# Performance work log

Hardware: AMD Instinct MI355X
Metric: run time of the kernel (lower is better)

## Reference

```python
import jax, jax.numpy as jnp
import numpy as np

N, E, IN_CH, HID, EDGE_DIM, L, G = 50000, 800000, 64, 128, 16, 3, 256

def _bn(h, g, b):
    # BatchNorm1d in training mode (biased batch variance), eps=1e-5
    m = h.mean(0)
    v = ((h - m) ** 2).mean(0)
    return (h - m) * jax.lax.rsqrt(v + 1e-5) * g + b

def setup_inputs() -> dict:
    key = jax.random.key(0)
    ks = jax.random.split(key, 24)
    s = 0.05
    inp = {
        'x': jax.random.normal(ks[0], (N, IN_CH), jnp.float32),
        'edge_attr': jax.random.uniform(ks[1], (E, EDGE_DIM), jnp.float32),
        'src': jax.random.randint(ks[2], (E,), 0, N, jnp.int32),
        'dst': jax.random.randint(ks[3], (E,), 0, N, jnp.int32),
        'batch': jnp.sort(jax.random.randint(ks[4], (N,), 0, G, jnp.int32)),
        'Wp': jax.random.normal(ks[5], (IN_CH, HID), jnp.float32) * s,
        'bp': jnp.zeros((HID,), jnp.float32),
        'conv_We': jax.random.normal(ks[6], (L, EDGE_DIM, HID), jnp.float32) * s,
        'conv_be': jnp.zeros((L, HID), jnp.float32),
        'conv_W1': jax.random.normal(ks[7], (L, HID, HID), jnp.float32) * s,
        'conv_b1': jnp.zeros((L, HID), jnp.float32),
        'conv_g1': jnp.ones((L, HID), jnp.float32),
        'conv_bt1': jnp.zeros((L, HID), jnp.float32),
        'conv_W2': jax.random.normal(ks[8], (L, HID, HID), jnp.float32) * s,
        'conv_b2': jnp.zeros((L, HID), jnp.float32),
        'bn_g': jnp.ones((L, HID), jnp.float32),
        'bn_b': jnp.zeros((L, HID), jnp.float32),
        'head_W1': jax.random.normal(ks[9], (HID * L * 2, HID), jnp.float32) * s,
        'head_b1': jnp.zeros((HID,), jnp.float32),
        'head_g': jnp.ones((HID,), jnp.float32),
        'head_bt': jnp.zeros((HID,), jnp.float32),
        'head_W2': jax.random.normal(ks[10], (HID, 1), jnp.float32) * s,
        'head_b2': jnp.zeros((1,), jnp.float32),
    }
    return inp

def reference(x, edge_attr, src, dst, batch, Wp, bp, conv_We, conv_be, conv_W1, conv_b1,
              conv_g1, conv_bt1, conv_W2, conv_b2, bn_g, bn_b, head_W1, head_b1,
              head_g, head_bt, head_W2, head_b2):
    n = x.shape[0]
    h = x @ Wp + bp  # [N, HID]
    outs = []
    for l in range(L):
        # GINEConv: msg = ReLU(x_src + lin(edge_attr)); sum-aggregate to dst; (1+eps)*x + agg, eps=0
        ee = edge_attr @ conv_We[l] + conv_be[l]          # [E, HID]
        msg = jax.nn.relu(h[src] + ee)                     # [E, HID]
        agg = jax.ops.segment_sum(msg, dst, num_segments=n)
        t = h + agg
        t = t @ conv_W1[l] + conv_b1[l]
        t = jax.nn.relu(_bn(t, conv_g1[l], conv_bt1[l]))
        t = t @ conv_W2[l] + conv_b2[l]
        h = jax.nn.relu(_bn(t, bn_g[l], bn_b[l]))          # outer BN + ReLU (dropout = identity, eval)
        outs.append(h)
    xj = jnp.concatenate(outs, axis=-1)                    # JK 'cat' -> [N, 3*HID]
    cnt = jax.ops.segment_sum(jnp.ones((n,), xj.dtype), batch, num_segments=G)
    z_mean = jax.ops.segment_sum(xj, batch, num_segments=G) / jnp.clip(cnt, 1.0)[:, None]
    z_max = jax.ops.segment_max(xj, batch, num_segments=G)
    z = jnp.concatenate([z_mean, z_max], axis=-1)          # [G, 6*HID]
    z = z @ head_W1 + head_b1
    z = jax.nn.relu(_bn(z, head_g, head_bt))
    return (z @ head_W2 + head_b2).squeeze(-1)             # [G]
```

## Files before the change

### kernel.cpp

```cpp
#include <hip/hip_runtime.h>
#include <hip/hip_bf16.h>

#define HID 128
#define EDIM 16

typedef float v4f __attribute__((ext_vector_type(4)));
typedef float v2f __attribute__((ext_vector_type(2)));
typedef short s8v __attribute__((ext_vector_type(8)));
typedef float f4v __attribute__((ext_vector_type(4)));

#define MFMA_BF16(a, b, c) __builtin_amdgcn_mfma_f32_16x16x32_bf16((a), (b), (c), 0, 0, 0)

__device__ __forceinline__ unsigned short bf16_rne(float v)
{
    unsigned u = __builtin_bit_cast(unsigned, v);
    return (unsigned short)((u + 0x7fffu + ((u >> 16) & 1u)) >> 16);
}

__device__ __forceinline__ unsigned pack2(float lo, float hi)
{
    return (unsigned)bf16_rne(lo) | ((unsigned)bf16_rne(hi) << 16);
}

__device__ __forceinline__ float bflo(unsigned u) { return __builtin_bit_cast(float, u << 16); }
__device__ __forceinline__ float bfhi(unsigned u) { return __builtin_bit_cast(float, u & 0xffff0000u); }

__device__ __forceinline__ v2f unpack2(unsigned u)
{
    v2f r; r.x = bflo(u); r.y = bfhi(u); return r;
}

__device__ __forceinline__ void split_bf16(float v, unsigned short& h, unsigned short& l)
{
    unsigned u = __builtin_bit_cast(unsigned, v);
    unsigned hu = (u + 0x7fffu + ((u >> 16) & 1u)) >> 16;
    h = (unsigned short)hu;
    float hf = __builtin_bit_cast(float, hu << 16);
    l = bf16_rne(v - hf);
}

__device__ __forceinline__ v2f vmax0(v2f a)
{
    v2f r; r.x = fmaxf(a.x, 0.f); r.y = fmaxf(a.y, 0.f); return r;
}

__global__ void hist_kernel(const int* __restrict__ dst, int* __restrict__ deg, int E)
{
    int e = blockIdx.x * 256 + threadIdx.x;
    if (e < E) atomicAdd(&deg[dst[e]], 1);
}

__global__ void block_sum_kernel(const int* __restrict__ deg, int* __restrict__ bsum, int Nn)
{
    int i = blockIdx.x * 256 + threadIdx.x;
    int v = (i < Nn) ? deg[i] : 0;
#pragma unroll
    for (int off = 32; off > 0; off >>= 1) v += __shfl_down(v, off, 64);
    __shared__ int ws[4];
    if ((threadIdx.x & 63) == 0) ws[threadIdx.x >> 6] = v;
    __syncthreads();
    if (threadIdx.x == 0) bsum[blockIdx.x] = ws[0] + ws[1] + ws[2] + ws[3];
}

__global__ void bsum_scan_kernel(int* bsum, int nb, int* total_out)
{
    __shared__ int sh[256];
    int tid = threadIdx.x;
    int v = (tid < nb) ? bsum[tid] : 0;
    sh[tid] = v;
    __syncthreads();
    for (int off = 1; off < 256; off <<= 1) {
        int tv = (tid >= off) ? sh[tid - off] : 0;
        __syncthreads();
        sh[tid] += tv;
        __syncthreads();
    }
    if (tid < nb) bsum[tid] = sh[tid] - v;
    if (tid == 255) *total_out = sh[255];
}

__global__ void block_scan_kernel(const int* __restrict__ deg, const int* __restrict__ bsum,
                                  int* __restrict__ row_start, int* __restrict__ cursor, int Nn)
{
    __shared__ int sh[256];
    int tid = threadIdx.x;
    int i = blockIdx.x * 256 + tid;
    int v = (i < Nn) ? deg[i] : 0;
    sh[tid] = v;
    __syncthreads();
    for (int off = 1; off < 256; off <<= 1) {
        int tv = (tid >= off) ? sh[tid - off] : 0;
        __syncthreads();
        sh[tid] += tv;
        __syncthreads();
    }
    if (i < Nn) {
        int excl = sh[tid] - v + bsum[blockIdx.x];
        row_start[i] = excl;
        cursor[i] = excl;
    }
}

__global__ void scatter_kernel(const int* __restrict__ src, const int* __restrict__ dst,
                               int* cursor, int* __restrict__ perm,
                               int* __restrict__ src_perm, int E)
{
    int e = blockIdx.x * 256 + threadIdx.x;
    if (e >= E) return;
    int pos = atomicAdd(&cursor[dst[e]], 1);
    perm[pos] = e;
    src_perm[pos] = src[e];
}

__global__ void gather_ea_kernel(const float* __restrict__ ea, const int* __restrict__ perm,
                                 float* __restrict__ ea_perm, int E)
{
    int idx = blockIdx.x * 256 + threadIdx.x;
    int p = idx >> 2, c = (idx & 3) * 4;
    if (p >= E) return;
    int e = perm[p];
    *(float4*)&ea_perm[(size_t)p * EDIM + c] = *(const float4*)&ea[(size_t)e * EDIM + c];
}

__global__ void prep_weights(const float* __restrict__ Wp, const float* __restrict__ W1,
                             const float* __restrict__ W2, unsigned short* __restrict__ out)
{
    int idx = blockIdx.x * 256 + threadIdx.x;
    if (idx < 8192) {
        int n = idx >> 6, k = idx & 63;
        unsigned short h, l;
        split_bf16(Wp[k * 128 + n], h, l);
        out[idx] = h;
        out[8192 + idx] = l;
    } else {
        int j = idx - 8192;
        if (j >= 6 * 16384) return;
        int m2 = j >> 14;
        int r = j & 16383;
        int n = r >> 7, k = r & 127;
        int l = m2 >> 1;
        const float* Wsrc = (m2 & 1) ? (W2 + l * 16384) : (W1 + l * 16384);
        unsigned short h, lo;
        split_bf16(Wsrc[k * 128 + n], h, lo);
        int base = 16384 + m2 * 32768;
        out[base + r] = h;
        out[base + 16384 + r] = lo;
    }
}

__device__ __forceinline__ void matvp(const v4f& a0, const v4f& a1,
                                      const v4f& a2, const v4f& a3,
                                      const v2f* __restrict__ w, v2f& m)
{
    m += w[0] * a0.x;  m += w[1] * a0.y;  m += w[2] * a0.z;  m += w[3] * a0.w;
    m += w[4] * a1.x;  m += w[5] * a1.y;  m += w[6] * a1.z;  m += w[7] * a1.w;
    m += w[8] * a2.x;  m += w[9] * a2.y;  m += w[10] * a2.z; m += w[11] * a2.w;
    m += w[12] * a3.x; m += w[13] * a3.y; m += w[14] * a3.z; m += w[15] * a3.w;
}

template<bool GATH>
__global__ __launch_bounds__(256, 8) void aggregate_kernel(
    const unsigned short* __restrict__ h16, const float* __restrict__ eaG,
    const int* __restrict__ perm, const int* __restrict__ src_perm,
    const int* __restrict__ row_start,
    const float* __restrict__ We, const float* __restrict__ be,
    float* __restrict__ t, int Nn)
{
    int tid = threadIdx.x;
    int lane = tid & 63;
    int c = lane * 2;
    v2f w[16];
#pragma unroll
    for (int k = 0; k < 16; ++k) w[k] = *(const v2f*)&We[k * HID + c];
    v2f bj = *(const v2f*)&be[c];
    int node = blockIdx.x * 4 + (tid >> 6);
    if (node >= Nn) return;
    const unsigned* __restrict__ hw = (const unsigned*)h16 + lane;
    v2f acc = unpack2(hw[(unsigned)node << 6]);
    int p0 = __builtin_amdgcn_readfirstlane(row_start[node]);
    int p1 = __builtin_amdgcn_readfirstlane(row_start[node + 1]);
    int p = p0;
    int s0 = 0, s1 = 0, s2 = 0, s3 = 0;
    if (p + 4 <= p1) { s0 = src_perm[p]; s1 = src_perm[p + 1]; s2 = src_perm[p + 2]; s3 = src_perm[p + 3]; }
    while (p + 4 <= p1) {
        int np = p + 4;
        int t0 = 0, t1 = 0, t2 = 0, t3 = 0;
        if (np + 4 <= p1) { t0 = src_perm[np]; t1 = src_perm[np + 1]; t2 = src_perm[np + 2]; t3 = src_perm[np + 3]; }
        unsigned hu0 = hw[(unsigned)s0 << 6];
        unsigned hu1 = hw[(unsigned)s1 << 6];
        unsigned hu2 = hw[(unsigned)s2 << 6];
        unsigned hu3 = hw[(unsigned)s3 << 6];
        int q0, q1, q2, q3;
        if (GATH) { q0 = p; q1 = p + 1; q2 = p + 2; q3 = p + 3; }
        else      { q0 = perm[p]; q1 = perm[p + 1]; q2 = perm[p + 2]; q3 = perm[p + 3]; }
        const v4f* e0 = (const v4f*)(eaG + (size_t)(unsigned)q0 * EDIM);
        const v4f* e1 = (const v4f*)(eaG + (size_t)(unsigned)q1 * EDIM);
        const v4f* e2 = (const v4f*)(eaG + (size_t)(unsigned)q2 * EDIM);
        const v4f* e3 = (const v4f*)(eaG + (size_t)(unsigned)q3 * EDIM);
        v4f a00 = e0[0], a01 = e0[1], a02 = e0[2], a03 = e0[3];
        v4f a10 = e1[0], a11 = e1[1], a12 = e1[2], a13 = e1[3];
        v4f a20 = e2[0], a21 = e2[1], a22 = e2[2], a23 = e2[3];
        v4f a30 = e3[0], a31 = e3[1], a32 = e3[2], a33 = e3[3];
        v2f m0 = bj + unpack2(hu0), m1 = bj + unpack2(hu1);
        v2f m2 = bj + unpack2(hu2), m3 = bj + unpack2(hu3);
        matvp(a00, a01, a02, a03, w, m0);
        matvp(a10, a11, a12, a13, w, m1);
        matvp(a20, a21, a22, a23, w, m2);
        matvp(a30, a31, a32, a33, w, m3);
        acc += vmax0(m0) + vmax0(m1) + vmax0(m2) + vmax0(m3);
        p = np;
        s0 = t0; s1 = t1; s2 = t2; s3 = t3;
    }
    for (; p < p1; ++p) {
        int s = src_perm[p];
        int q = GATH ? p : perm[p];
        const v4f* e0 = (const v4f*)(eaG + (size_t)(unsigned)q * EDIM);
        v4f a0 = e0[0], a1 = e0[1], a2 = e0[2], a3 = e0[3];
        v2f m0 = bj + unpack2(hw[(unsigned)s << 6]);
        matvp(a0, a1, a2, a3, w, m0);
        acc += vmax0(m0);
    }
    *(v2f*)(t + ((unsigned)node << 7) + c) = acc;
}

#define LPAD 40

template<int K, bool PRE_BN, bool POST_STATS, bool OUT_BF16>
__global__ __launch_bounds__(256) void gemm_mfma(
    const float* __restrict__ A, const unsigned short* __restrict__ Wh,
    const unsigned short* __restrict__ Wl, const float* __restrict__ bias,
    const float* __restrict__ preStats, const float* __restrict__ preG, const float* __restrict__ preB,
    void* __restrict__ Cout, float* __restrict__ postStats, int Nrows, float invN)
{
    __shared__ __align__(16) unsigned short Ah[128 * LPAD], Al[128 * LPAD];
    __shared__ __align__(16) unsigned short Bh[128 * LPAD], Bl[128 * LPAD];
    __shared__ float sc[PRE_BN ? K : 1], sb[PRE_BN ? K : 1];
    int tid = threadIdx.x;
    int rbase = blockIdx.x * 128;
    if (PRE_BN) {
        if (tid < K) {
            float mean = preStats[tid] * invN;
            float var = preStats[K + tid] * invN - mean * mean;
            float rstd = rsqrtf(var + 1e-5f);
            float g = preG[tid];
            sc[tid] = rstd * g;
            sb[tid] = preB[tid] - mean * rstd * g;
        }
        __syncthreads();
    }
    int w = tid >> 6, nl = tid & 15, q = (tid >> 4) & 3;
    f4v acc[2][8];
#pragma unroll
    for (int mt = 0; mt < 2; ++mt)
#pragma unroll
        for (int nt = 0; nt < 8; ++nt)
#pragma unroll
            for (int r = 0; r < 4; ++r) acc[mt][nt][r] = 0.f;

    for (int ks = 0; ks < K / 32; ++ks) {
        int k0 = ks * 32;
        if (ks) __syncthreads();
#pragma unroll
        for (int i = 0; i < 4; ++i) {
            int cidx = tid + i * 256;
            int m = cidx >> 3, k4 = (cidx & 7) * 4;
            int gr = rbase + m;
            float4 v = make_float4(0.f, 0.f, 0.f, 0.f);
            if (gr < Nrows) v = *(const float4*)&A[(size_t)gr * K + k0 + k4];
            if (PRE_BN) {
                v.x = fmaxf(v.x * sc[k0 + k4]     + sb[k0 + k4],     0.f);
                v.y = fmaxf(v.y * sc[k0 + k4 + 1] + sb[k0 + k4 + 1], 0.f);
                v.z = fmaxf(v.z * sc[k0 + k4 + 2] + sb[k0 + k4 + 2], 0.f);
                v.w = fmaxf(v.w * sc[k0 + k4 + 3] + sb[k0 + k4 + 3], 0.f);
            }
            unsigned short h0, l0, h1, l1, h2, l2, h3, l3;
            split_bf16(v.x, h0, l0); split_bf16(v.y, h1, l1);
            split_bf16(v.z, h2, l2); split_bf16(v.w, h3, l3);
            uint2 hp, lp;
            hp.x = (unsigned)h0 | ((unsigned)h1 << 16); hp.y = (unsigned)h2 | ((unsigned)h3 << 16);
            lp.x = (unsigned)l0 | ((unsigned)l1 << 16); lp.y = (unsigned)l2 | ((unsigned)l3 << 16);
            *(uint2*)&Ah[m * LPAD + k4] = hp;
            *(uint2*)&Al[m * LPAD + k4] = lp;
        }
#pragma unroll
        for (int i = 0; i < 2; ++i) {
            int g = tid + i * 256;
            int n = g >> 2, kq = (g & 3) * 8;
            uint4 hv = *(const uint4*)&Wh[(size_t)n * K + k0 + kq];
            uint4 lv = *(const uint4*)&Wl[(size_t)n * K + k0 + kq];
            *(uint4*)&Bh[n * LPAD + kq] = hv;
            *(uint4*)&Bl[n * LPAD + kq] = lv;
        }
        __syncthreads();
        s8v ah0 = *(const s8v*)&Ah[(w * 32 + nl) * LPAD + q * 8];
        s8v ah1 = *(const s8v*)&Ah[(w * 32 + 16 + nl) * LPAD + q * 8];
        s8v al0 = *(const s8v*)&Al[(w * 32 + nl) * LPAD + q * 8];
        s8v al1 = *(const s8v*)&Al[(w * 32 + 16 + nl) * LPAD + q * 8];
#pragma unroll
        for (int nt = 0; nt < 8; ++nt) {
            s8v bh = *(const s8v*)&Bh[(nt * 16 + nl) * LPAD + q * 8];
            s8v bl = *(const s8v*)&Bl[(nt * 16 + nl) * LPAD + q * 8];
            acc[0][nt] = MFMA_BF16(ah0, bh, acc[0][nt]);
            acc[0][nt] = MFMA_BF16(ah0, bl, acc[0][nt]);
            acc[0][nt] = MFMA_BF16(al0, bh, acc[0][nt]);
            acc[1][nt] = MFMA_BF16(ah1, bh, acc[1][nt]);
            acc[1][nt] = MFMA_BF16(ah1, bl, acc[1][nt]);
            acc[1][nt] = MFMA_BF16(al1, bh, acc[1][nt]);
        }
    }
    __syncthreads();

    float* Cf = (float*)Cout;
    unsigned short* Ch = (unsigned short*)Cout;
    float* redS = (float*)Ah;
    float* redQ = (float*)Al;
#pragma unroll
    for (int nt = 0; nt < 8; ++nt) {
        int col = nt * 16 + nl;
        float bcol = bias[col];
        float sv = 0.f, qv = 0.f;
#pragma unroll
        for (int mt = 0; mt < 2; ++mt) {
#pragma unroll
            for (int r = 0; r < 4; ++r) {
                int grow = rbase + w * 32 + mt * 16 + q * 4 + r;
                if (grow < Nrows) {
                    float o = acc[mt][nt][r] + bcol;
                    if (OUT_BF16) Ch[(size_t)grow * HID + col] = bf16_rne(o);
                    else          Cf[(size_t)grow * HID + col] = o;
                    if (POST_STATS) { sv += o; qv += o * o; }
                }
            }
        }
        if (POST_STATS) {
            sv += __shfl_down(sv, 32, 64); sv += __shfl_down(sv, 16, 64);
            qv += __shfl_down(qv, 32, 64); qv += __shfl_down(qv, 16, 64);
            if ((tid & 63) < 16) { redS[w * 128 + col] = sv; redQ[w * 128 + col] = qv; }
        }
    }
    if (POST_STATS) {
        __syncthreads();
        if (tid < 128) {
            float S = redS[tid] + redS[128 + tid] + redS[256 + tid] + redS[384 + tid];
            float Q = redQ[tid] + redQ[128 + tid] + redQ[256 + tid] + redQ[384 + tid];
            atomicAdd(&postStats[tid], S);
            atomicAdd(&postStats[128 + tid], Q);
        }
    }
}

__global__ void bn_apply_pool(const float* __restrict__ X, unsigned short* __restrict__ h16,
                              const float* __restrict__ stats, const float* __restrict__ g,
                              const float* __restrict__ b, const int* __restrict__ starts,
                              float* __restrict__ z, int l, float invN)
{
    int gph = blockIdx.x;
    int tid = threadIdx.x;
    int ch4 = (tid & 31) * 4, wk = tid >> 5;
    float sc[4], sh[4];
#pragma unroll
    for (int u = 0; u < 4; ++u) {
        int j = ch4 + u;
        float mean = stats[j] * invN;
        float var = stats[128 + j] * invN - mean * mean;
        float rstd = rsqrtf(var + 1e-5f);
        float gg = g[j];
        sc[u] = rstd * gg;
        sh[u] = b[j] - mean * rstd * gg;
    }
    int s = starts[gph], e = starts[gph + 1];
    float4 sum = make_float4(0.f, 0.f, 0.f, 0.f);
    float4 mx = make_float4(0.f, 0.f, 0.f, 0.f);
    unsigned* hv32 = (unsigned*)h16;
    for (int n = s + wk; n < e; n += 16) {
        float4 v = *(const float4*)&X[(size_t)n * HID + ch4];
        v.x = fmaxf(v.x * sc[0] + sh[0], 0.f);
        v.y = fmaxf(v.y * sc[1] + sh[1], 0.f);
        v.z = fmaxf(v.z * sc[2] + sh[2], 0.f);
        v.w = fmaxf(v.w * sc[3] + sh[3], 0.f);
        uint2 pk;
        pk.x = pack2(v.x, v.y);
        pk.y = pack2(v.z, v.w);
        *(uint2*)&hv32[(size_t)n * 64 + (ch4 >> 1)] = pk;
        sum.x += v.x; sum.y += v.y; sum.z += v.z; sum.w += v.w;
        mx.x = fmaxf(mx.x, v.x); mx.y = fmaxf(mx.y, v.y);
        mx.z = fmaxf(mx.z, v.z); mx.w = fmaxf(mx.w, v.w);
    }
    __shared__ float ls[16 * 128], lm[16 * 128];
    *(float4*)&ls[wk * 128 + ch4] = sum;
    *(float4*)&lm[wk * 128 + ch4] = mx;
    __syncthreads();
    if (tid < 128) {
        float S = 0.f, M = 0.f;
#pragma unroll
        for (int k = 0; k < 16; ++k) {
            S += ls[k * 128 + tid];
            M = fmaxf(M, lm[k * 128 + tid]);
        }
        float cnt = (float)(e - s);
        z[(size_t)gph * 768 + l * 128 + tid] = S / fmaxf(cnt, 1.f);
        z[(size_t)gph * 768 + 384 + l * 128 + tid] = M;
    }
}

__global__ void starts_kernel(const int* __restrict__ batch, int* __restrict__ starts,
                              int Nn, int Gn)
{
    int g = blockIdx.x * blockDim.x + threadIdx.x;
    if (g > Gn) return;
    int lo = 0, hi = Nn;
    while (lo < hi) { int mid = (lo + hi) >> 1; if (batch[mid] < g) lo = mid + 1; else hi = mid; }
    starts[g] = lo;
}

__global__ void head_gemm1(const float* __restrict__ z, const float* __restrict__ W,
                           const float* __restrict__ bias, float* __restrict__ zr,
                           float* __restrict__ msums)
{
    __shared__ __align__(16) float zl[768];
    int g = blockIdx.x, j = threadIdx.x;
    for (int i = j; i < 768; i += 128) zl[i] = z[(size_t)g * 768 + i];
    __syncthreads();
    float acc = bias[j];
    for (int k = 0; k < 768; k += 4) {
        float4 a4 = *(const float4*)&zl[k];
        acc += a4.x * W[k * 128 + j] + a4.y * W[(k + 1) * 128 + j]
             + a4.z * W[(k + 2) * 128 + j] + a4.w * W[(k + 3) * 128 + j];
    }
    zr[(size_t)g * 128 + j] = acc;
    atomicAdd(&msums[j], acc);
    atomicAdd(&msums[128 + j], acc * acc);
}

__global__ void head_final(const float* __restrict__ zr, const float* __restrict__ msums,
                           const float* __restrict__ hg, const float* __restrict__ hb,
                           const float* __restrict__ W2, const float* __restrict__ b2,
                           float* __restrict__ out, float invG)
{
    int g = blockIdx.x, j = threadIdx.x;
    float mean = msums[j] * invG;
    float var = msums[128 + j] * invG - mean * mean;
    float rstd = rsqrtf(var + 1e-5f);
    float v = zr[(size_t)g * 128 + j];
    v = (v - mean) * rstd * hg[j] + hb[j];
    v = fmaxf(v, 0.f);
    float p = v * W2[j];
#pragma unroll
    for (int off = 32; off > 0; off >>= 1) p += __shfl_down(p, off, 64);
    __shared__ float partial[2];
    if ((j & 63) == 0) partial[j >> 6] = p;
    __syncthreads();
    if (j == 0) out[g] = partial[0] + partial[1] + b2[0];
}

extern "C" void kernel_launch(void* const* d_in, const int* in_sizes, int n_in,
                              void* d_out, int out_size, void* d_ws, size_t ws_size,
                              hipStream_t stream)
{
    const float* x         = (const float*)d_in[0];
    const float* edge_attr = (const float*)d_in[1];
    const int*   src       = (const int*)d_in[2];
    const int*   dst       = (const int*)d_in[3];
    const int*   batch     = (const int*)d_in[4];
    const float* Wp        = (const float*)d_in[5];
    const float* bp        = (const float*)d_in[6];
    const float* conv_We   = (const float*)d_in[7];
    const float* conv_be   = (const float*)d_in[8];
    const float* conv_W1   = (const float*)d_in[9];
    const float* conv_b1   = (const float*)d_in[10];
    const float* conv_g1   = (const float*)d_in[11];
    const float* conv_bt1  = (const float*)d_in[12];
    const float* conv_W2   = (const float*)d_in[13];
    const float* conv_b2   = (const float*)d_in[14];
    const float* bn_g      = (const float*)d_in[15];
    const float* bn_b      = (const float*)d_in[16];
    const float* head_W1   = (const float*)d_in[17];
    const float* head_b1   = (const float*)d_in[18];
    const float* head_g    = (const float*)d_in[19];
    const float* head_bt   = (const float*)d_in[20];
    const float* head_W2   = (const float*)d_in[21];
    const float* head_b2   = (const float*)d_in[22];

    const int N = in_sizes[4];
    const int E = in_sizes[2];
    const int G = out_size;
    const int L = 3;

    float* t        = (float*)d_ws;
    unsigned short* h16 = (unsigned short*)(t + (size_t)N * HID);
    float* z        = (float*)(h16 + (size_t)N * HID);
    float* zr       = z + (size_t)G * 768;
    float* statsAll = zr + (size_t)G * HID;
    int*   deg      = (int*)(statsAll + 7 * 256);
    int*   starts   = deg + N;
    int*   row_start= starts + (G + 1);
    int*   cursor   = row_start + (N + 1);
    int*   bsum     = cursor + N;
    int*   src_perm = bsum + 256;
    int*   perm     = src_perm + E;
    unsigned short* wt = (unsigned short*)(perm + E);
    size_t base_end = (size_t)((char*)(wt + 212992) - (char*)d_ws);
    size_t ea_off = (base_end + 63) & ~(size_t)63;
    bool gath = (ea_off + (size_t)E * EDIM * sizeof(float)) <= ws_size;
    float* ea_perm = (float*)((char*)d_ws + ea_off);
    float* msums = statsAll + 6 * 256;

    (void)n_in;

    const float invN = 1.0f / (float)N;
    const float invG = 1.0f / (float)G;
    const int nb = (N + 255) / 256;
    const int gemmBlocks = (N + 127) / 128;

    (void)hipMemsetAsync(statsAll, 0, 7 * 256 * sizeof(float) + (size_t)N * sizeof(int), stream);
    hist_kernel<<<(E + 255) / 256, 256, 0, stream>>>(dst, deg, E);
    block_sum_kernel<<<nb, 256, 0, stream>>>(deg, bsum, N);
    bsum_scan_kernel<<<1, 256, 0, stream>>>(bsum, nb, &row_start[N]);
    block_scan_kernel<<<nb, 256, 0, stream>>>(deg, bsum, row_start, cursor, N);
    scatter_kernel<<<(E + 255) / 256, 256, 0, stream>>>(src, dst, cursor, perm, src_perm, E);
    if (gath)
        gather_ea_kernel<<<(E * 4 + 255) / 256, 256, 0, stream>>>(edge_attr, perm, ea_perm, E);
    starts_kernel<<<1, 512, 0, stream>>>(batch, starts, N, G);
    prep_weights<<<(8192 + 6 * 16384 + 255) / 256, 256, 0, stream>>>(Wp, conv_W1, conv_W2, wt);

    const unsigned short* Wp_hi = wt;
    const unsigned short* Wp_lo = wt + 8192;

    gemm_mfma<64, false, false, true><<<gemmBlocks, 256, 0, stream>>>(
        x, Wp_hi, Wp_lo, bp, nullptr, nullptr, nullptr, h16, nullptr, N, invN);

    for (int l = 0; l < L; ++l) {
        float* sI = statsAll + l * 512;
        float* sO = sI + 256;
        const unsigned short* W1hi = wt + 16384 + (size_t)(2 * l) * 32768;
        const unsigned short* W1lo = W1hi + 16384;
        const unsigned short* W2hi = wt + 16384 + (size_t)(2 * l + 1) * 32768;
        const unsigned short* W2lo = W2hi + 16384;
        if (gath)
            aggregate_kernel<true><<<(N + 3) / 4, 256, 0, stream>>>(
                h16, ea_perm, perm, src_perm, row_start,
                conv_We + (size_t)l * EDIM * HID, conv_be + l * HID, t, N);
        else
            aggregate_kernel<false><<<(N + 3) / 4, 256, 0, stream>>>(
                h16, edge_attr, perm, src_perm, row_start,
                conv_We + (size_t)l * EDIM * HID, conv_be + l * HID, t, N);
        gemm_mfma<128, false, true, false><<<gemmBlocks, 256, 0, stream>>>(
            t, W1hi, W1lo, conv_b1 + l * HID,
            nullptr, nullptr, nullptr, t, sI, N, invN);
        gemm_mfma<128, true, true, false><<<gemmBlocks, 256, 0, stream>>>(
            t, W2hi, W2lo, conv_b2 + l * HID,
            sI, conv_g1 + l * HID, conv_bt1 + l * HID, t, sO, N, invN);
        bn_apply_pool<<<G, 512, 0, stream>>>(
            t, h16, sO, bn_g + l * HID, bn_b + l * HID, starts, z, l, invN);
    }

    head_gemm1<<<G, 128, 0, stream>>>(z, head_W1, head_b1, zr, msums);
    head_final<<<G, 128, 0, stream>>>(zr, msums, head_g, head_bt, head_W2, head_b2,
                                      (float*)d_out, invG);
}
```

Measured before the change: 675.1 us.

## Stage per-wave edge attributes and source indices in LDS for aggregation

The aggregation kernel now loads each node's edge_attr rows and source indices in chunks of 64 into per-wave shared memory with coalesced float4 loads. Previously every lane re-read the same edge_attr rows as broadcast global loads. The inner loop reads edge features from LDS and prefetches neighbour h values two groups ahead through the staged index buffer. It adds about 20KB of LDS per block and lowers the occupancy hint from 8 to 4. No barriers are used, so correctness relies on implicit wave-level ordering of the LDS writes and reads.

```diff
diff --git a/kernel.cpp b/kernel.cpp
--- a/kernel.cpp
+++ b/kernel.cpp
@@ -159,66 +159,114 @@
 }
 
 template<bool GATH>
-__global__ __launch_bounds__(256, 8) void aggregate_kernel(
+__global__ __launch_bounds__(256, 4) void aggregate_kernel(
     const unsigned short* __restrict__ h16, const float* __restrict__ eaG,
     const int* __restrict__ perm, const int* __restrict__ src_perm,
     const int* __restrict__ row_start,
     const float* __restrict__ We, const float* __restrict__ be,
-    float* __restrict__ t, int Nn)
-{
+    float* __restrict__ t, int Nn, int Etot)
+{
+    __shared__ __align__(16) float ea_s[4][64 * EDIM];
+    __shared__ __align__(16) int   src_s[4][72];
+    __shared__ __align__(16) int   perm_s[4][64];
+
     int tid = threadIdx.x;
-    int lane = tid & 63;
+    int w = tid >> 6, lane = tid & 63;
     int c = lane * 2;
-    v2f w[16];
-#pragma unroll
-    for (int k = 0; k < 16; ++k) w[k] = *(const v2f*)&We[k * HID + c];
+    v2f wv[16];
+#pragma unroll
+    for (int k = 0; k < 16; ++k) wv[k] = *(const v2f*)&We[k * HID + c];
     v2f bj = *(const v2f*)&be[c];
-    int node = blockIdx.x * 4 + (tid >> 6);
+    int node = blockIdx.x * 4 + w;
     if (node >= Nn) return;
     const unsigned* __restrict__ hw = (const unsigned*)h16 + lane;
     v2f acc = unpack2(hw[(unsigned)node << 6]);
     int p0 = __builtin_amdgcn_readfirstlane(row_start[node]);
     int p1 = __builtin_amdgcn_readfirstlane(row_start[node + 1]);
-    int p = p0;
-    int s0 = 0, s1 = 0, s2 = 0, s3 = 0;
-    if (p + 4 <= p1) { s0 = src_perm[p]; s1 = src_perm[p + 1]; s2 = src_perm[p + 2]; s3 = src_perm[p + 3]; }
-    while (p + 4 <= p1) {
-        int np = p + 4;
-        int t0 = 0, t1 = 0, t2 = 0, t3 = 0;
-        if (np + 4 <= p1) { t0 = src_perm[np]; t1 = src_perm[np + 1]; t2 = src_perm[np + 2]; t3 = src_perm[np + 3]; }
-        unsigned hu0 = hw[(unsigned)s0 << 6];
-        unsigned hu1 = hw[(unsigned)s1 << 6];
-        unsigned hu2 = hw[(unsigned)s2 << 6];
-        unsigned hu3 = hw[(unsigned)s3 << 6];
-        int q0, q1, q2, q3;
-        if (GATH) { q0 = p; q1 = p + 1; q2 = p + 2; q3 = p + 3; }
-        else      { q0 = perm[p]; q1 = perm[p + 1]; q2 = perm[p + 2]; q3 = perm[p + 3]; }
-        const v4f* e0 = (const v4f*)(eaG + (size_t)(unsigned)q0 * EDIM);
-        const v4f* e1 = (const v4f*)(eaG + (size_t)(unsigned)q1 * EDIM);
-        const v4f* e2 = (const v4f*)(eaG + (size_t)(unsigned)q2 * EDIM);
-        const v4f* e3 = (const v4f*)(eaG + (size_t)(unsigned)q3 * EDIM);
-        v4f a00 = e0[0], a01 = e0[1], a02 = e0[2], a03 = e0[3];
-        v4f a10 = e1[0], a11 = e1[1], a12 = e1[2], a13 = e1[3];
-        v4f a20 = e2[0], a21 = e2[1], a22 = e2[2], a23 = e2[3];
-        v4f a30 = e3[0], a31 = e3[1], a32 = e3[2], a33 = e3[3];
-        v2f m0 = bj + unpack2(hu0), m1 = bj + unpack2(hu1);
-        v2f m2 = bj + unpack2(hu2), m3 = bj + unpack2(hu3);
-        matvp(a00, a01, a02, a03, w, m0);
-        matvp(a10, a11, a12, a13, w, m1);
-        matvp(a20, a21, a22, a23, w, m2);
-        matvp(a30, a31, a32, a33, w, m3);
-        acc += vmax0(m0) + vmax0(m1) + vmax0(m2) + vmax0(m3);
-        p = np;
-        s0 = t0; s1 = t1; s2 = t2; s3 = t3;
-    }
-    for (; p < p1; ++p) {
-        int s = src_perm[p];
-        int q = GATH ? p : perm[p];
-        const v4f* e0 = (const v4f*)(eaG + (size_t)(unsigned)q * EDIM);
-        v4f a0 = e0[0], a1 = e0[1], a2 = e0[2], a3 = e0[3];
-        v2f m0 = bj + unpack2(hw[(unsigned)s << 6]);
-        matvp(a0, a1, a2, a3, w, m0);
-        acc += vmax0(m0);
+    float* eas = ea_s[w];
+    int*   srcs = src_s[w];
+    int*   prms = perm_s[w];
+
+    for (int cs = p0; cs < p1; cs += 64) {
+        int cn = p1 - cs; if (cn > 64) cn = 64;
+
+        srcs[lane] = (cs + lane < p1) ? src_perm[cs + lane] : 0;
+        if (lane < 8) srcs[64 + lane] = 0;
+
+        if (GATH) {
+#pragma unroll
+            for (int tp = 0; tp < 4; ++tp) {
+                if (tp * 16 < cn) {
+                    int e = cs + tp * 16 + (lane >> 2);
+                    float4 v = make_float4(0.f, 0.f, 0.f, 0.f);
+                    if (e < Etot) v = *(const float4*)&eaG[(size_t)e * EDIM + (lane & 3) * 4];
+                    *(float4*)&eas[tp * 256 + lane * 4] = v;
+                }
+            }
+        } else {
+            prms[lane] = (cs + lane < p1) ? perm[cs + lane] : 0;
+#pragma unroll
+            for (int tp = 0; tp < 4; ++tp) {
+                if (tp * 16 < cn) {
+                    int el = tp * 16 + (lane >> 2);
+                    int pv = prms[el];
+                    float4 v = *(const float4*)&eaG[(size_t)(unsigned)pv * EDIM + (lane & 3) * 4];
+                    *(float4*)&eas[tp * 256 + lane * 4] = v;
+                }
+            }
+        }
+
+        int ngroups = (cn + 3) >> 2;
+        int4 scur = *(const int4*)&srcs[0];
+        int4 snxt = *(const int4*)&srcs[4];
+        unsigned hu0 = hw[(unsigned)scur.x << 6];
+        unsigned hu1 = hw[(unsigned)scur.y << 6];
+        unsigned hu2 = hw[(unsigned)scur.z << 6];
+        unsigned hu3 = hw[(unsigned)scur.w << 6];
+        for (int g = 0; g < ngroups; ++g) {
+            int4 s2 = *(const int4*)&srcs[(g + 2) * 4];
+            unsigned hn0 = hw[(unsigned)snxt.x << 6];
+            unsigned hn1 = hw[(unsigned)snxt.y << 6];
+            unsigned hn2 = hw[(unsigned)snxt.z << 6];
+            unsigned hn3 = hw[(unsigned)snxt.w << 6];
+            int eb = g * 4;
+            v4f a0 = *(const v4f*)&eas[(eb + 0) * EDIM + 0];
+            v4f a1 = *(const v4f*)&eas[(eb + 0) * EDIM + 4];
+            v4f a2 = *(const v4f*)&eas[(eb + 0) * EDIM + 8];
+            v4f a3 = *(const v4f*)&eas[(eb + 0) * EDIM + 12];
+            v2f m0 = bj + unpack2(hu0);
+            matvp(a0, a1, a2, a3, wv, m0);
+            a0 = *(const v4f*)&eas[(eb + 1) * EDIM + 0];
+            a1 = *(const v4f*)&eas[(eb + 1) * EDIM + 4];
+            a2 = *(const v4f*)&eas[(eb + 1) * EDIM + 8];
+            a3 = *(const v4f*)&eas[(eb + 1) * EDIM + 12];
+            v2f m1 = bj + unpack2(hu1);
+            matvp(a0, a1, a2, a3, wv, m1);
+            a0 = *(const v4f*)&eas[(eb + 2) * EDIM + 0];
+            a1 = *(const v4f*)&eas[(eb + 2) * EDIM + 4];
+            a2 = *(const v4f*)&eas[(eb + 2) * EDIM + 8];
+            a3 = *(const v4f*)&eas[(eb + 2) * EDIM + 12];
+            v2f m2 = bj + unpack2(hu2);
+            matvp(a0, a1, a2, a3, wv, m2);
+            a0 = *(const v4f*)&eas[(eb + 3) * EDIM + 0];
+            a1 = *(const v4f*)&eas[(eb + 3) * EDIM + 4];
+            a2 = *(const v4f*)&eas[(eb + 3) * EDIM + 8];
+            a3 = *(const v4f*)&eas[(eb + 3) * EDIM + 12];
+            v2f m3 = bj + unpack2(hu3);
+            matvp(a0, a1, a2, a3, wv, m3);
+
+            v2f r0 = vmax0(m0), r1 = vmax0(m1), r2 = vmax0(m2), r3 = vmax0(m3);
+            if (eb + 4 <= cn) {
+                acc += (r0 + r1) + (r2 + r3);
+            } else {
+                if (eb + 0 < cn) acc += r0;
+                if (eb + 1 < cn) acc += r1;
+                if (eb + 2 < cn) acc += r2;
+                if (eb + 3 < cn) acc += r3;
+            }
+            hu0 = hn0; hu1 = hn1; hu2 = hn2; hu3 = hn3;
+            scur = snxt; snxt = s2;
+        }
     }
     *(v2f*)(t + ((unsigned)node << 7) + c) = acc;
 }
@@ -539,11 +587,11 @@
         if (gath)
             aggregate_kernel<true><<<(N + 3) / 4, 256, 0, stream>>>(
                 h16, ea_perm, perm, src_perm, row_start,
-                conv_We + (size_t)l * EDIM * HID, conv_be + l * HID, t, N);
+                conv_We + (size_t)l * EDIM * HID, conv_be + l * HID, t, N, E);
         else
             aggregate_kernel<false><<<(N + 3) / 4, 256, 0, stream>>>(
                 h16, edge_attr, perm, src_perm, row_start,
-                conv_We + (size_t)l * EDIM * HID, conv_be + l * HID, t, N);
+                conv_We + (size_t)l * EDIM * HID, conv_be + l * HID, t, N, E);
         gemm_mfma<128, false, true, false><<<gemmBlocks, 256, 0, stream>>>(
             t, W1hi, W1lo, conv_b1 + l * HID,
             nullptr, nullptr, nullptr, t, sI, N, invN);
```

New measurement: 716.8 us. +6.2%, slower.

## Compute edge linear in aggregation with bf16 MFMA instead of scalar FMAs

Applied to the files above, without the earlier changes.

Replaces the per-lane scalar 16x128 edge-attribute projection in the GINE aggregation with MFMA 16x16x32 bf16 ops over 16-edge chunks. Edge attributes are split into hi/lo bf16 pairs, the bias is folded in as an extra K column, and the weights are pre-transposed to bf16 by a new prep kernel. It then gathers source features as scalar bf16 loads, masks padded rows, and reduces partial sums across lanes through shared memory. The aim is to cut VALU work per edge. In exchange it adds narrower gathers, wasted MFMA work on low-degree nodes, a lower occupancy hint, and bf16 rounding of the weights.

```diff
diff --git a/kernel.cpp b/kernel.cpp
--- a/kernel.cpp
+++ b/kernel.cpp
@@ -37,11 +37,6 @@
     h = (unsigned short)hu;
     float hf = __builtin_bit_cast(float, hu << 16);
     l = bf16_rne(v - hf);
-}
-
-__device__ __forceinline__ v2f vmax0(v2f a)
-{
-    v2f r; r.x = fmaxf(a.x, 0.f); r.y = fmaxf(a.y, 0.f); return r;
 }
 
 __global__ void hist_kernel(const int* __restrict__ dst, int* __restrict__ deg, int E)
@@ -148,79 +143,119 @@
     }
 }
 
-__device__ __forceinline__ void matvp(const v4f& a0, const v4f& a1,
-                                      const v4f& a2, const v4f& a3,
-                                      const v2f* __restrict__ w, v2f& m)
-{
-    m += w[0] * a0.x;  m += w[1] * a0.y;  m += w[2] * a0.z;  m += w[3] * a0.w;
-    m += w[4] * a1.x;  m += w[5] * a1.y;  m += w[6] * a1.z;  m += w[7] * a1.w;
-    m += w[8] * a2.x;  m += w[9] * a2.y;  m += w[10] * a2.z; m += w[11] * a2.w;
-    m += w[12] * a3.x; m += w[13] * a3.y; m += w[14] * a3.z; m += w[15] * a3.w;
+__global__ void prep_wet(const float* __restrict__ We, const float* __restrict__ be,
+                         unsigned short* __restrict__ out)
+{
+    int idx = blockIdx.x * 256 + threadIdx.x;
+    if (idx >= 3 * 4096) return;
+    int l = idx >> 12, r = idx & 4095, ch = r >> 5, k = r & 31;
+    float v = 0.f;
+    if (k < 16)       v = We[l * EDIM * HID + k * HID + ch];
+    else if (k == 16) v = be[l * HID + ch];
+    out[idx] = bf16_rne(v);
 }
 
 template<bool GATH>
-__global__ __launch_bounds__(256, 8) void aggregate_kernel(
+__global__ __launch_bounds__(256, 4) void aggregate_kernel(
     const unsigned short* __restrict__ h16, const float* __restrict__ eaG,
     const int* __restrict__ perm, const int* __restrict__ src_perm,
-    const int* __restrict__ row_start,
-    const float* __restrict__ We, const float* __restrict__ be,
+    const int* __restrict__ row_start, const unsigned short* __restrict__ WeT,
     float* __restrict__ t, int Nn)
 {
+    __shared__ float fin_s[4][132];
     int tid = threadIdx.x;
-    int lane = tid & 63;
-    int c = lane * 2;
-    v2f w[16];
-#pragma unroll
-    for (int k = 0; k < 16; ++k) w[k] = *(const v2f*)&We[k * HID + c];
-    v2f bj = *(const v2f*)&be[c];
-    int node = blockIdx.x * 4 + (tid >> 6);
+    int w = tid >> 6, lane = tid & 63;
+    int qq = lane >> 4, m16 = lane & 15;
+
+    int node = blockIdx.x * 4 + w;
     if (node >= Nn) return;
-    const unsigned* __restrict__ hw = (const unsigned*)h16 + lane;
-    v2f acc = unpack2(hw[(unsigned)node << 6]);
+
+    s8v bf[8];
+#pragma unroll
+    for (int nt = 0; nt < 8; ++nt)
+        bf[nt] = *(const s8v*)&WeT[(size_t)((nt * 16 + m16) * 32 + qq * 8)];
+
+    v2f selfpair = unpack2(((const unsigned*)h16)[((unsigned)node << 6) + lane]);
+
     int p0 = __builtin_amdgcn_readfirstlane(row_start[node]);
     int p1 = __builtin_amdgcn_readfirstlane(row_start[node + 1]);
-    int p = p0;
-    int s0 = 0, s1 = 0, s2 = 0, s3 = 0;
-    if (p + 4 <= p1) { s0 = src_perm[p]; s1 = src_perm[p + 1]; s2 = src_perm[p + 2]; s3 = src_perm[p + 3]; }
-    while (p + 4 <= p1) {
-        int np = p + 4;
-        int t0 = 0, t1 = 0, t2 = 0, t3 = 0;
-        if (np + 4 <= p1) { t0 = src_perm[np]; t1 = src_perm[np + 1]; t2 = src_perm[np + 2]; t3 = src_perm[np + 3]; }
-        unsigned hu0 = hw[(unsigned)s0 << 6];
-        unsigned hu1 = hw[(unsigned)s1 << 6];
-        unsigned hu2 = hw[(unsigned)s2 << 6];
-        unsigned hu3 = hw[(unsigned)s3 << 6];
-        int q0, q1, q2, q3;
-        if (GATH) { q0 = p; q1 = p + 1; q2 = p + 2; q3 = p + 3; }
-        else      { q0 = perm[p]; q1 = perm[p + 1]; q2 = perm[p + 2]; q3 = perm[p + 3]; }
-        const v4f* e0 = (const v4f*)(eaG + (size_t)(unsigned)q0 * EDIM);
-        const v4f* e1 = (const v4f*)(eaG + (size_t)(unsigned)q1 * EDIM);
-        const v4f* e2 = (const v4f*)(eaG + (size_t)(unsigned)q2 * EDIM);
-        const v4f* e3 = (const v4f*)(eaG + (size_t)(unsigned)q3 * EDIM);
-        v4f a00 = e0[0], a01 = e0[1], a02 = e0[2], a03 = e0[3];
-        v4f a10 = e1[0], a11 = e1[1], a12 = e1[2], a13 = e1[3];
-        v4f a20 = e2[0], a21 = e2[1], a22 = e2[2], a23 = e2[3];
-        v4f a30 = e3[0], a31 = e3[1], a32 = e3[2], a33 = e3[3];
-        v2f m0 = bj + unpack2(hu0), m1 = bj + unpack2(hu1);
-        v2f m2 = bj + unpack2(hu2), m3 = bj + unpack2(hu3);
-        matvp(a00, a01, a02, a03, w, m0);
-        matvp(a10, a11, a12, a13, w, m1);
-        matvp(a20, a21, a22, a23, w, m2);
-        matvp(a30, a31, a32, a33, w, m3);
-        acc += vmax0(m0) + vmax0(m1) + vmax0(m2) + vmax0(m3);
-        p = np;
-        s0 = t0; s1 = t1; s2 = t2; s3 = t3;
-    }
-    for (; p < p1; ++p) {
-        int s = src_perm[p];
-        int q = GATH ? p : perm[p];
-        const v4f* e0 = (const v4f*)(eaG + (size_t)(unsigned)q * EDIM);
-        v4f a0 = e0[0], a1 = e0[1], a2 = e0[2], a3 = e0[3];
-        v2f m0 = bj + unpack2(hw[(unsigned)s << 6]);
-        matvp(a0, a1, a2, a3, w, m0);
-        acc += vmax0(m0);
-    }
-    *(v2f*)(t + ((unsigned)node << 7) + c) = acc;
+
+    float acc8[8] = {0.f, 0.f, 0.f, 0.f, 0.f, 0.f, 0.f, 0.f};
+
+    for (int cs = p0; cs < p1; cs += 16) {
+        int cn = p1 - cs; if (cn > 16) cn = 16;
+
+        s8v ah = {0, 0, 0, 0, 0, 0, 0, 0};
+        s8v al = {0, 0, 0, 0, 0, 0, 0, 0};
+        if (lane < 48) {
+            if (lane < 32) {
+                int er = cs + m16;
+                if (er < p1) {
+                    int rowi = GATH ? er : perm[er];
+                    const float* ap = &eaG[(size_t)(unsigned)rowi * EDIM + qq * 8];
+                    float4 f0 = *(const float4*)ap;
+                    float4 f1 = *(const float4*)(ap + 4);
+                    unsigned short hh, ll;
+                    split_bf16(f0.x, hh, ll); ah[0] = (short)hh; al[0] = (short)ll;
+                    split_bf16(f0.y, hh, ll); ah[1] = (short)hh; al[1] = (short)ll;
+                    split_bf16(f0.z, hh, ll); ah[2] = (short)hh; al[2] = (short)ll;
+                    split_bf16(f0.w, hh, ll); ah[3] = (short)hh; al[3] = (short)ll;
+                    split_bf16(f1.x, hh, ll); ah[4] = (short)hh; al[4] = (short)ll;
+                    split_bf16(f1.y, hh, ll); ah[5] = (short)hh; al[5] = (short)ll;
+                    split_bf16(f1.z, hh, ll); ah[6] = (short)hh; al[6] = (short)ll;
+                    split_bf16(f1.w, hh, ll); ah[7] = (short)hh; al[7] = (short)ll;
+                }
+            } else {
+                ah[0] = (short)0x3F80;
+            }
+        }
+
+        int ii = cs + 4 * qq;
+        int sv0 = (ii     < p1) ? src_perm[ii]     : 0;
+        int sv1 = (ii + 1 < p1) ? src_perm[ii + 1] : 0;
+        int sv2 = (ii + 2 < p1) ? src_perm[ii + 2] : 0;
+        int sv3 = (ii + 3 < p1) ? src_perm[ii + 3] : 0;
+        float msk0 = (4 * qq + 0 < cn) ? 1.f : 0.f;
+        float msk1 = (4 * qq + 1 < cn) ? 1.f : 0.f;
+        float msk2 = (4 * qq + 2 < cn) ? 1.f : 0.f;
+        float msk3 = (4 * qq + 3 < cn) ? 1.f : 0.f;
+
+#pragma unroll
+        for (int hf = 0; hf < 2; ++hf) {
+            unsigned short hA[4][4];
+#pragma unroll
+            for (int k = 0; k < 4; ++k) {
+                int cb = (hf * 4 + k) * 16 + m16;
+                hA[k][0] = h16[(size_t)(unsigned)sv0 * HID + cb];
+                hA[k][1] = h16[(size_t)(unsigned)sv1 * HID + cb];
+                hA[k][2] = h16[(size_t)(unsigned)sv2 * HID + cb];
+                hA[k][3] = h16[(size_t)(unsigned)sv3 * HID + cb];
+            }
+#pragma unroll
+            for (int k = 0; k < 4; ++k) {
+                int nt = hf * 4 + k;
+                f4v d = {0.f, 0.f, 0.f, 0.f};
+                d = MFMA_BF16(ah, bf[nt], d);
+                d = MFMA_BF16(al, bf[nt], d);
+                acc8[nt] += fmaxf(d[0] + bflo((unsigned)hA[k][0]), 0.f) * msk0
+                          + fmaxf(d[1] + bflo((unsigned)hA[k][1]), 0.f) * msk1
+                          + fmaxf(d[2] + bflo((unsigned)hA[k][2]), 0.f) * msk2
+                          + fmaxf(d[3] + bflo((unsigned)hA[k][3]), 0.f) * msk3;
+            }
+        }
+    }
+
+    float* fin = &fin_s[w][0];
+#pragma unroll
+    for (int nt = 0; nt < 8; ++nt) {
+        float v = acc8[nt];
+        v += __shfl_xor(v, 16, 64);
+        v += __shfl_xor(v, 32, 64);
+        if (lane < 16) fin[nt * 16 + lane] = v;
+    }
+    v2f r2 = *(v2f*)&fin[2 * lane];
+    v2f outv; outv.x = r2.x + selfpair.x; outv.y = r2.y + selfpair.y;
+    *(v2f*)(t + ((unsigned)node << 7) + 2 * lane) = outv;
 }
 
 #define LPAD 40
@@ -499,7 +534,7 @@
     int*   src_perm = bsum + 256;
     int*   perm     = src_perm + E;
     unsigned short* wt = (unsigned short*)(perm + E);
-    size_t base_end = (size_t)((char*)(wt + 212992) - (char*)d_ws);
+    size_t base_end = (size_t)((char*)(wt + 212992 + 3 * 4096) - (char*)d_ws);
     size_t ea_off = (base_end + 63) & ~(size_t)63;
     bool gath = (ea_off + (size_t)E * EDIM * sizeof(float)) <= ws_size;
     float* ea_perm = (float*)((char*)d_ws + ea_off);
@@ -522,6 +557,7 @@
         gather_ea_kernel<<<(E * 4 + 255) / 256, 256, 0, stream>>>(edge_attr, perm, ea_perm, E);
     starts_kernel<<<1, 512, 0, stream>>>(batch, starts, N, G);
     prep_weights<<<(8192 + 6 * 16384 + 255) / 256, 256, 0, stream>>>(Wp, conv_W1, conv_W2, wt);
+    prep_wet<<<(3 * 4096 + 255) / 256, 256, 0, stream>>>(conv_We, conv_be, wt + 212992);
 
     const unsigned short* Wp_hi = wt;
     const unsigned short* Wp_lo = wt + 8192;
@@ -536,14 +572,13 @@
         const unsigned short* W1lo = W1hi + 16384;
         const unsigned short* W2hi = wt + 16384 + (size_t)(2 * l + 1) * 32768;
         const unsigned short* W2lo = W2hi + 16384;
+        const unsigned short* wet_l = wt + 212992 + (size_t)l * 4096;
         if (gath)
             aggregate_kernel<true><<<(N + 3) / 4, 256, 0, stream>>>(
-                h16, ea_perm, perm, src_perm, row_start,
-                conv_We + (size_t)l * EDIM * HID, conv_be + l * HID, t, N);
+                h16, ea_perm, perm, src_perm, row_start, wet_l, t, N);
         else
             aggregate_kernel<false><<<(N + 3) / 4, 256, 0, stream>>>(
-                h16, edge_attr, perm, src_perm, row_start,
-                conv_We + (size_t)l * EDIM * HID, conv_be + l * HID, t, N);
+                h16, edge_attr, perm, src_perm, row_start, wet_l, t, N);
         gemm_mfma<128, false, true, false><<<gemmBlocks, 256, 0, stream>>>(
             t, W1hi, W1lo, conv_b1 + l * HID,
             nullptr, nullptr, nullptr, t, sI, N, invN);
```

New measurement: 759.2 us. +12.5%, slower.

## Store permuted edge attributes in fp16 and use dot2 in aggregation

Applied to the files above, without the earlier changes.

The edge-attribute gather now converts attributes to packed fp16, which halves their storage and read traffic. The aggregation kernel computes the edge linear layer with fdot2 packed-half dot products against fp16-packed weights held in registers. The main loop is unrolled to 8 edges and prefetches the next source features one iteration ahead. Quantising edge attributes and weights to fp16 reduces accuracy, and the deeper prefetch raises register pressure.

```diff
diff --git a/kernel.cpp b/kernel.cpp
--- a/kernel.cpp
+++ b/kernel.cpp
@@ -1,5 +1,6 @@
 #include <hip/hip_runtime.h>
 #include <hip/hip_bf16.h>
+#include <hip/hip_fp16.h>
 
 #define HID 128
 #define EDIM 16
@@ -8,6 +9,8 @@
 typedef float v2f __attribute__((ext_vector_type(2)));
 typedef short s8v __attribute__((ext_vector_type(8)));
 typedef float f4v __attribute__((ext_vector_type(4)));
+typedef unsigned int u8x __attribute__((ext_vector_type(8)));
+typedef _Float16 h2v __attribute__((ext_vector_type(2)));
 
 #define MFMA_BF16(a, b, c) __builtin_amdgcn_mfma_f32_16x16x32_bf16((a), (b), (c), 0, 0, 0)
 
@@ -42,6 +45,18 @@
 __device__ __forceinline__ v2f vmax0(v2f a)
 {
     v2f r; r.x = fmaxf(a.x, 0.f); r.y = fmaxf(a.y, 0.f); return r;
+}
+
+__device__ __forceinline__ unsigned pkh2(float lo, float hi)
+{
+    return (unsigned)__half_as_ushort(__float2half(lo)) |
+           ((unsigned)__half_as_ushort(__float2half(hi)) << 16);
+}
+
+__device__ __forceinline__ void dot2(float& d, unsigned ea, unsigned w)
+{
+    d = __builtin_amdgcn_fdot2(__builtin_bit_cast(h2v, ea),
+                               __builtin_bit_cast(h2v, w), d, false);
 }
 
 __global__ void hist_kernel(const int* __restrict__ dst, int* __restrict__ deg, int E)
@@ -112,14 +127,22 @@
     src_perm[pos] = src[e];
 }
 
-__global__ void gather_ea_kernel(const float* __restrict__ ea, const int* __restrict__ perm,
-                                 float* __restrict__ ea_perm, int E)
+__global__ void gather_ea_f16(const float* __restrict__ ea, const int* __restrict__ perm,
+                              unsigned* __restrict__ eaH, int E)
 {
     int idx = blockIdx.x * 256 + threadIdx.x;
-    int p = idx >> 2, c = (idx & 3) * 4;
+    int p = idx >> 1, hf = idx & 1;
     if (p >= E) return;
     int e = perm[p];
-    *(float4*)&ea_perm[(size_t)p * EDIM + c] = *(const float4*)&ea[(size_t)e * EDIM + c];
+    const float* ap = &ea[(size_t)e * EDIM + hf * 8];
+    float4 f0 = *(const float4*)ap;
+    float4 f1 = *(const float4*)(ap + 4);
+    uint4 o;
+    o.x = pkh2(f0.x, f0.y);
+    o.y = pkh2(f0.z, f0.w);
+    o.z = pkh2(f1.x, f1.y);
+    o.w = pkh2(f1.z, f1.w);
+    *(uint4*)&eaH[(size_t)p * 8 + hf * 4] = o;
 }
 
 __global__ void prep_weights(const float* __restrict__ Wp, const float* __restrict__ W1,
@@ -148,6 +171,97 @@
     }
 }
 
+__device__ __forceinline__ void edge_f16(v2f& acc, v2f bj, unsigned hu, const u8x& e,
+                                         const unsigned* __restrict__ wpk0,
+                                         const unsigned* __restrict__ wpk1)
+{
+    float m0 = bj.x + bflo(hu);
+    float m1 = bj.y + bfhi(hu);
+#pragma unroll
+    for (int kp = 0; kp < 8; ++kp) {
+        dot2(m0, e[kp], wpk0[kp]);
+        dot2(m1, e[kp], wpk1[kp]);
+    }
+    acc.x += fmaxf(m0, 0.f);
+    acc.y += fmaxf(m1, 0.f);
+}
+
+__global__ __launch_bounds__(256, 8) void aggregate_f16(
+    const unsigned short* __restrict__ h16, const unsigned* __restrict__ eaH,
+    const int* __restrict__ src_perm, const int* __restrict__ row_start,
+    const float* __restrict__ We, const float* __restrict__ be,
+    float* __restrict__ t, int Nn)
+{
+    int tid = threadIdx.x;
+    int lane = tid & 63;
+    int c = lane * 2;
+    unsigned wpk0[8], wpk1[8];
+#pragma unroll
+    for (int kp = 0; kp < 8; ++kp) {
+        wpk0[kp] = pkh2(We[(2 * kp) * HID + c],     We[(2 * kp + 1) * HID + c]);
+        wpk1[kp] = pkh2(We[(2 * kp) * HID + c + 1], We[(2 * kp + 1) * HID + c + 1]);
+    }
+    v2f bj = *(const v2f*)&be[c];
+    int node = blockIdx.x * 4 + (tid >> 6);
+    if (node >= Nn) return;
+    const unsigned* __restrict__ hw = (const unsigned*)h16 + lane;
+    v2f acc = unpack2(hw[(unsigned)node << 6]);
+    int p0 = __builtin_amdgcn_readfirstlane(row_start[node]);
+    int p1 = __builtin_amdgcn_readfirstlane(row_start[node + 1]);
+    int p = p0;
+
+    int s0 = 0, s1 = 0, s2 = 0, s3 = 0, s4 = 0, s5 = 0, s6 = 0, s7 = 0;
+    unsigned hu0 = 0, hu1 = 0, hu2 = 0, hu3 = 0, hu4 = 0, hu5 = 0, hu6 = 0, hu7 = 0;
+    if (p + 8 <= p1) {
+        s0 = src_perm[p];     s1 = src_perm[p + 1]; s2 = src_perm[p + 2]; s3 = src_perm[p + 3];
+        s4 = src_perm[p + 4]; s5 = src_perm[p + 5]; s6 = src_perm[p + 6]; s7 = src_perm[p + 7];
+        hu0 = hw[(unsigned)s0 << 6]; hu1 = hw[(unsigned)s1 << 6];
+        hu2 = hw[(unsigned)s2 << 6]; hu3 = hw[(unsigned)s3 << 6];
+        hu4 = hw[(unsigned)s4 << 6]; hu5 = hw[(unsigned)s5 << 6];
+        hu6 = hw[(unsigned)s6 << 6]; hu7 = hw[(unsigned)s7 << 6];
+    }
+    while (p + 8 <= p1) {
+        int np = p + 8;
+        u8x e0 = *(const u8x*)(eaH + (size_t)(unsigned)(p    ) * 8);
+        u8x e1 = *(const u8x*)(eaH + (size_t)(unsigned)(p + 1) * 8);
+        u8x e2 = *(const u8x*)(eaH + (size_t)(unsigned)(p + 2) * 8);
+        u8x e3 = *(const u8x*)(eaH + (size_t)(unsigned)(p + 3) * 8);
+        u8x e4 = *(const u8x*)(eaH + (size_t)(unsigned)(p + 4) * 8);
+        u8x e5 = *(const u8x*)(eaH + (size_t)(unsigned)(p + 5) * 8);
+        u8x e6 = *(const u8x*)(eaH + (size_t)(unsigned)(p + 6) * 8);
+        u8x e7 = *(const u8x*)(eaH + (size_t)(unsigned)(p + 7) * 8);
+        int t0 = 0, t1 = 0, t2 = 0, t3 = 0, t4 = 0, t5 = 0, t6 = 0, t7 = 0;
+        unsigned hn0 = 0, hn1 = 0, hn2 = 0, hn3 = 0, hn4 = 0, hn5 = 0, hn6 = 0, hn7 = 0;
+        if (np + 8 <= p1) {
+            t0 = src_perm[np];     t1 = src_perm[np + 1]; t2 = src_perm[np + 2]; t3 = src_perm[np + 3];
+            t4 = src_perm[np + 4]; t5 = src_perm[np + 5]; t6 = src_perm[np + 6]; t7 = src_perm[np + 7];
+            hn0 = hw[(unsigned)t0 << 6]; hn1 = hw[(unsigned)t1 << 6];
+            hn2 = hw[(unsigned)t2 << 6]; hn3 = hw[(unsigned)t3 << 6];
+            hn4 = hw[(unsigned)t4 << 6]; hn5 = hw[(unsigned)t5 << 6];
+            hn6 = hw[(unsigned)t6 << 6]; hn7 = hw[(unsigned)t7 << 6];
+        }
+        edge_f16(acc, bj, hu0, e0, wpk0, wpk1);
+        edge_f16(acc, bj, hu1, e1, wpk0, wpk1);
+        edge_f16(acc, bj, hu2, e2, wpk0, wpk1);
+        edge_f16(acc, bj, hu3, e3, wpk0, wpk1);
+        edge_f16(acc, bj, hu4, e4, wpk0, wpk1);
+        edge_f16(acc, bj, hu5, e5, wpk0, wpk1);
+        edge_f16(acc, bj, hu6, e6, wpk0, wpk1);
+        edge_f16(acc, bj, hu7, e7, wpk0, wpk1);
+        p = np;
+        s0 = t0; s1 = t1; s2 = t2; s3 = t3; s4 = t4; s5 = t5; s6 = t6; s7 = t7;
+        hu0 = hn0; hu1 = hn1; hu2 = hn2; hu3 = hn3;
+        hu4 = hn4; hu5 = hn5; hu6 = hn6; hu7 = hn7;
+    }
+    for (; p < p1; ++p) {
+        int s = src_perm[p];
+        unsigned hu = hw[(unsigned)s << 6];
+        u8x e = *(const u8x*)(eaH + (size_t)(unsigned)p * 8);
+        edge_f16(acc, bj, hu, e, wpk0, wpk1);
+    }
+    *(v2f*)(t + ((unsigned)node << 7) + c) = acc;
+}
+
 __device__ __forceinline__ void matvp(const v4f& a0, const v4f& a1,
                                       const v4f& a2, const v4f& a3,
                                       const v2f* __restrict__ w, v2f& m)
@@ -158,8 +272,7 @@
     m += w[12] * a3.x; m += w[13] * a3.y; m += w[14] * a3.z; m += w[15] * a3.w;
 }
 
-template<bool GATH>
-__global__ __launch_bounds__(256, 8) void aggregate_kernel(
+__global__ __launch_bounds__(256, 8) void aggregate_fp32(
     const unsigned short* __restrict__ h16, const float* __restrict__ eaG,
     const int* __restrict__ perm, const int* __restrict__ src_perm,
     const int* __restrict__ row_start,
@@ -190,9 +303,7 @@
         unsigned hu1 = hw[(unsigned)s1 << 6];
         unsigned hu2 = hw[(unsigned)s2 << 6];
         unsigned hu3 = hw[(unsigned)s3 << 6];
-        int q0, q1, q2, q3;
-        if (GATH) { q0 = p; q1 = p + 1; q2 = p + 2; q3 = p + 3; }
-        else      { q0 = perm[p]; q1 = perm[p + 1]; q2 = perm[p + 2]; q3 = perm[p + 3]; }
+        int q0 = perm[p], q1 = perm[p + 1], q2 = perm[p + 2], q3 = perm[p + 3];
         const v4f* e0 = (const v4f*)(eaG + (size_t)(unsigned)q0 * EDIM);
         const v4f* e1 = (const v4f*)(eaG + (size_t)(unsigned)q1 * EDIM);
         const v4f* e2 = (const v4f*)(eaG + (size_t)(unsigned)q2 * EDIM);
@@ -207,13 +318,13 @@
         matvp(a10, a11, a12, a13, w, m1);
         matvp(a20, a21, a22, a23, w, m2);
         matvp(a30, a31, a32, a33, w, m3);
-        acc += vmax0(m0) + vmax0(m1) + vmax0(m2) + vmax0(m3);
+        acc += (vmax0(m0) + vmax0(m1)) + (vmax0(m2) + vmax0(m3));
         p = np;
         s0 = t0; s1 = t1; s2 = t2; s3 = t3;
     }
     for (; p < p1; ++p) {
         int s = src_perm[p];
-        int q = GATH ? p : perm[p];
+        int q = perm[p];
         const v4f* e0 = (const v4f*)(eaG + (size_t)(unsigned)q * EDIM);
         v4f a0 = e0[0], a1 = e0[1], a2 = e0[2], a3 = e0[3];
         v2f m0 = bj + unpack2(hw[(unsigned)s << 6]);
@@ -501,8 +612,8 @@
     unsigned short* wt = (unsigned short*)(perm + E);
     size_t base_end = (size_t)((char*)(wt + 212992) - (char*)d_ws);
     size_t ea_off = (base_end + 63) & ~(size_t)63;
-    bool gath = (ea_off + (size_t)E * EDIM * sizeof(float)) <= ws_size;
-    float* ea_perm = (float*)((char*)d_ws + ea_off);
+    bool gath = (ea_off + (size_t)E * 8 * sizeof(unsigned)) <= ws_size;
+    unsigned* eaH = (unsigned*)((char*)d_ws + ea_off);
     float* msums = statsAll + 6 * 256;
 
     (void)n_in;
@@ -519,7 +630,7 @@
     block_scan_kernel<<<nb, 256, 0, stream>>>(deg, bsum, row_start, cursor, N);
     scatter_kernel<<<(E + 255) / 256, 256, 0, stream>>>(src, dst, cursor, perm, src_perm, E);
     if (gath)
-        gather_ea_kernel<<<(E * 4 + 255) / 256, 256, 0, stream>>>(edge_attr, perm, ea_perm, E);
+        gather_ea_f16<<<(E * 2 + 255) / 256, 256, 0, stream>>>(edge_attr, perm, eaH, E);
     starts_kernel<<<1, 512, 0, stream>>>(batch, starts, N, G);
     prep_weights<<<(8192 + 6 * 16384 + 255) / 256, 256, 0, stream>>>(Wp, conv_W1, conv_W2, wt);
 
@@ -537,11 +648,11 @@
         const unsigned short* W2hi = wt + 16384 + (size_t)(2 * l + 1) * 32768;
         const unsigned short* W2lo = W2hi + 16384;
         if (gath)
-            aggregate_kernel<true><<<(N + 3) / 4, 256, 0, stream>>>(
-                h16, ea_perm, perm, src_perm, row_start,
+            aggregate_f16<<<(N + 3) / 4, 256, 0, stream>>>(
+                h16, eaH, src_perm, row_start,
                 conv_We + (size_t)l * EDIM * HID, conv_be + l * HID, t, N);
         else
-            aggregate_kernel<false><<<(N + 3) / 4, 256, 0, stream>>>(
+            aggregate_fp32<<<(N + 3) / 4, 256, 0, stream>>>(
                 h16, edge_attr, perm, src_perm, row_start,
                 conv_We + (size_t)l * EDIM * HID, conv_be + l * HID, t, N);
         gemm_mfma<128, false, true, false><<<gemmBlocks, 256, 0, stream>>>(
```

Measured after the change: 669.2 us. About the same (-0.9%).
